# Kernel tuning notes

Hardware: AMD Instinct MI355X
Metric: run time of the kernel (lower is better)

Reference implementation:

```python
import jax, jax.numpy as jnp
import numpy as np

K = 128      # classes
CIN = 128    # ch_in
CL = 128     # ch_latent
B, H, W = 8, 1, 8192
SLOPE = 0.01 # F.leaky_relu default
EPS = 1e-5   # BatchNorm eps


def lrelu(x):
    return jnp.where(x >= 0, x, SLOPE * x)


def conv1x1(x, w, b):
    # x: (B,C,H,W), w: (O,C), b: (O,)
    return jnp.einsum('bchw,oc->bohw', x, w) + b[None, :, None, None]


def bn_eval(x, gamma, beta, mean, var):
    scale = gamma * jax.lax.rsqrt(var + EPS)
    return x * scale[None, :, None, None] + (beta - mean * scale)[None, :, None, None]


def setup_inputs() -> dict:
    key = jax.random.key(0)
    ks = jax.random.split(key, 16)
    def w(k, shape, fan_in):
        return jax.random.normal(k, shape, jnp.float32) / np.sqrt(fan_in)
    return {
        'x_in': jax.random.normal(ks[0], (B, CIN, H, W), jnp.float32),
        'cl1_w': w(ks[1], (CL, CIN), CIN), 'cl1_b': jnp.zeros((CL,), jnp.float32),
        'bn1_gamma': jnp.ones((CL,), jnp.float32), 'bn1_beta': jnp.zeros((CL,), jnp.float32),
        'bn1_mean': 0.1 * jax.random.normal(ks[2], (CL,), jnp.float32),
        'bn1_var': jax.random.uniform(ks[3], (CL,), jnp.float32, 0.5, 1.5),
        'cl2_w': w(ks[4], (CL, CL), CL), 'cl2_b': jnp.zeros((CL,), jnp.float32),
        'cl3_w': w(ks[5], (K + 1, CL), CL), 'cl3_b': jnp.zeros((K + 1,), jnp.float32),
        'reg1_w': w(ks[6], (CL, CIN), CIN), 'reg1_b': jnp.zeros((CL,), jnp.float32),
        'bnr_gamma': jnp.ones((CL,), jnp.float32), 'bnr_beta': jnp.zeros((CL,), jnp.float32),
        'bnr_mean': 0.1 * jax.random.normal(ks[7], (CL,), jnp.float32),
        'bnr_var': jax.random.uniform(ks[8], (CL,), jnp.float32, 0.5, 1.5),
        'cm2_w': w(ks[9], (K, CL, 32), CL), 'cm2_b': jnp.zeros((K, 32), jnp.float32),
        'cm3_w': w(ks[10], (K, 32, 1), 32), 'cm3_b': jnp.zeros((K, 1), jnp.float32),
    }


def reference(x_in, cl1_w, cl1_b, bn1_gamma, bn1_beta, bn1_mean, bn1_var,
              cl2_w, cl2_b, cl3_w, cl3_b,
              reg1_w, reg1_b, bnr_gamma, bnr_beta, bnr_mean, bnr_var,
              cm2_w, cm2_b, cm3_w, cm3_b):
    # classification branch
    x = lrelu(bn_eval(conv1x1(x_in, cl1_w, cl1_b), bn1_gamma, bn1_beta, bn1_mean, bn1_var))
    x = lrelu(conv1x1(x, cl2_w, cl2_b))
    x = conv1x1(x, cl3_w, cl3_b)                    # (B, K+1, H, W)
    logits = x[:, :K]
    mask = lrelu(x[:, -1:])                          # (B,1,H,W)
    inds = jnp.argmax(logits, axis=1)                # (B,H,W) int
    inds_r = inds.reshape(-1).astype(jnp.int32)      # (N,)
    xr = lrelu(bn_eval(conv1x1(x_in, reg1_w, reg1_b), bnr_gamma, bnr_beta, bnr_mean, bnr_var))
    # torch: transpose(1,3).reshape(-1, C)  -> (B,W,H,C) flatten
    xr = jnp.transpose(xr, (0, 3, 2, 1)).reshape(-1, CL)   # (N, CL)
    # CondMul 1: per-pixel gathered weight (N,CL,32)
    h = lrelu(jnp.einsum('ni,nio->no', xr, cm2_w[inds_r]) + cm2_b[inds_r])
    # CondMul 2: (N,32)->(N,1)
    reg = jnp.einsum('ni,nio->no', h, cm3_w[inds_r]) + cm3_b[inds_r]
    reg = reg.reshape(B, 1, 1, -1)                   # (B,1,1,H*W)
    x_real = (inds[:, None].astype(jnp.float32) + reg) * (1.0 / K)
    return x_real, mask
```

## Files before the change

kernel.cpp:

```cpp
#include <hip/hip_runtime.h>
#include <math.h>

#define NPOS 65536
#define NCH  128
#define DELTA 0.008f
#define HPAD 16

#define OFF_XR   0u
#define OFF_W1T  8388608u
#define OFF_W2T  (OFF_W1T + 16384u)
#define OFF_W3T  (OFF_W2T + 16384u)
#define OFF_B1F  (OFF_W3T + 16384u)
#define OFF_BRF  (OFF_B1F + 128u)
#define OFF_B2F  (OFF_BRF + 128u)
#define OFF_B3F  (OFF_B2F + 128u)
#define OFF_BF16 (OFF_B3F + 132u)
#define OFF_INT  (OFF_BF16 + 329728u)

#define UW1H 0u
#define UW1L 16384u
#define UWRH 32768u
#define UWRL 49152u
#define UW2H 65536u
#define UW2L 81920u
#define UW3H 98304u
#define UW3L 116736u
#define UW2K 135168u

#define NST 2080

typedef short bf16x8 __attribute__((ext_vector_type(8)));
typedef float f32x4 __attribute__((ext_vector_type(4)));
#define MFMA16 __builtin_amdgcn_mfma_f32_16x16x32_bf16

__device__ __forceinline__ float lrelu(float v) { return v >= 0.0f ? v : 0.01f * v; }
__device__ __forceinline__ unsigned short f2bf(float f) {
    unsigned u = __float_as_uint(f);
    return (unsigned short)((u + 0x7fffu + ((u >> 16) & 1u)) >> 16);
}
__device__ __forceinline__ float bf2f(unsigned short h) {
    return __uint_as_float(((unsigned)h) << 16);
}
__device__ __forceinline__ unsigned long long pack4(unsigned short a, unsigned short b,
                                                    unsigned short c, unsigned short d) {
    return (unsigned long long)a | ((unsigned long long)b << 16)
         | ((unsigned long long)c << 32) | ((unsigned long long)d << 48);
}

__global__ void k_prep(const float* __restrict__ cl1_w, const float* __restrict__ cl1_b,
                       const float* __restrict__ g1, const float* __restrict__ be1,
                       const float* __restrict__ mu1, const float* __restrict__ va1,
                       const float* __restrict__ cl2_w, const float* __restrict__ cl2_b,
                       const float* __restrict__ cl3_w, const float* __restrict__ cl3_b,
                       const float* __restrict__ reg1_w, const float* __restrict__ reg1_b,
                       const float* __restrict__ gr, const float* __restrict__ ber,
                       const float* __restrict__ mur, const float* __restrict__ var_,
                       const float* __restrict__ cm2w,
                       float* __restrict__ ws_f, unsigned short* __restrict__ wbf,
                       int* __restrict__ hist, int* __restrict__ cur,
                       int* __restrict__ fixcnt)
{
    const int bid = blockIdx.x;
    const int t = threadIdx.x;
    if (bid >= 128) {
        __shared__ float tl[32 * 132];
        int k = bid - 128;
        #pragma unroll
        for (int i = 0; i < 32; ++i) {
            float v = cm2w[(unsigned)k * 4096u + i * 128 + t];
            int ci = i * 4 + (t >> 5), o = t & 31;
            tl[o * 132 + ci] = v;
        }
        __syncthreads();
        #pragma unroll
        for (int i = 0; i < 32; ++i)
            wbf[UW2K + (unsigned)k * 4096u + i * 128 + t] = f2bf(tl[i * 132 + t]);
        return;
    }
    const int cout = bid;
    const int cin = t;
    const int row = cout * 128 + cin;
    float s1 = g1[cout] / sqrtf(va1[cout] + 1e-5f);
    float sr = gr[cout] / sqrtf(var_[cout] + 1e-5f);
    float w1 = cl1_w[row] * s1;
    float wr = reg1_w[row] * sr;
    float w2 = cl2_w[row];
    float w3 = cl3_w[row];
    ws_f[OFF_W1T + cin * 128 + cout] = w1;
    ws_f[OFF_W2T + cin * 128 + cout] = w2;
    ws_f[OFF_W3T + cin * 128 + cout] = w3;
    unsigned short h;
    h = f2bf(w1); wbf[UW1H + row] = h; wbf[UW1L + row] = f2bf(w1 - bf2f(h));
    h = f2bf(wr); wbf[UWRH + row] = h; wbf[UWRL + row] = f2bf(wr - bf2f(h));
    h = f2bf(w2); wbf[UW2H + row] = h; wbf[UW2L + row] = f2bf(w2 - bf2f(h));
    h = f2bf(w3); wbf[UW3H + row] = h; wbf[UW3L + row] = f2bf(w3 - bf2f(h));
    if (bid < 16) {
        float v = (bid == 0) ? cl3_w[128 * 128 + t] : 0.0f;
        int jj = (128 + bid) * 128 + t;
        h = f2bf(v); wbf[UW3H + jj] = h; wbf[UW3L + jj] = f2bf(v - bf2f(h));
    }
    if (bid == 0) {
        float s1b = g1[t] / sqrtf(va1[t] + 1e-5f);
        float srb = gr[t] / sqrtf(var_[t] + 1e-5f);
        ws_f[OFF_B1F + t] = cl1_b[t] * s1b + be1[t] - mu1[t] * s1b;
        ws_f[OFF_BRF + t] = reg1_b[t] * srb + ber[t] - mur[t] * srb;
        ws_f[OFF_B2F + t] = cl2_b[t];
        ws_f[OFF_B3F + t] = cl3_b[t];
        hist[t * HPAD] = 0;
        cur[t * HPAD] = 0;
    }
    if (bid == 1 && t == 0) { ws_f[OFF_B3F + 128] = cl3_b[128]; fixcnt[0] = 0; }
}

__global__ __launch_bounds__(256, 4)
void k_fused(const float* __restrict__ X, const float* __restrict__ wsf,
             const unsigned short* __restrict__ wbf,
             unsigned short* __restrict__ XRB, float* __restrict__ out_mask,
             int* __restrict__ inds, int* __restrict__ hist,
             int* __restrict__ fixcnt, int* __restrict__ fixlist)
{
    __shared__ __align__(16) unsigned short XBh[64 * 136];
    __shared__ __align__(16) unsigned short XBl[64 * 136];
    __shared__ float sm1[4 * 64];
    __shared__ float sm2[4 * 64];
    __shared__ int   si1[4 * 64];
    __shared__ int   lh[128];

    const int t = threadIdx.x;
    const int lane = t & 63;
    const int cl16 = lane & 15;
    const int q8 = (lane >> 4) * 8;
    const int q4 = (lane >> 4) * 4;
    const int wv = __builtin_amdgcn_readfirstlane(t >> 6);
    const unsigned nt64 = blockIdx.x * 64u;
    const unsigned base = nt64 + (nt64 >> 13) * 1040384u;

    const unsigned short* W1H = wbf + UW1H; const unsigned short* W1L = wbf + UW1L;
    const unsigned short* WRH = wbf + UWRH; const unsigned short* WRL = wbf + UWRL;
    const unsigned short* W2H = wbf + UW2H; const unsigned short* W2L = wbf + UW2L;
    const unsigned short* W3H = wbf + UW3H; const unsigned short* W3L = wbf + UW3L;
    const float* b1f = wsf + OFF_B1F;
    const float* brf = wsf + OFF_BRF;
    const float* b2f = wsf + OFF_B2F;
    const float* b3f = wsf + OFF_B3F;

    const f32x4 vzero = {0.f, 0.f, 0.f, 0.f};

    {
        const int pos = t & 63, cig = t >> 6;
        #pragma unroll
        for (int l = 0; l < 8; ++l) {
            int ci0 = cig * 32 + l * 4;
            float v0 = X[base + (unsigned)(ci0 + 0) * 8192u + pos];
            float v1 = X[base + (unsigned)(ci0 + 1) * 8192u + pos];
            float v2 = X[base + (unsigned)(ci0 + 2) * 8192u + pos];
            float v3 = X[base + (unsigned)(ci0 + 3) * 8192u + pos];
            unsigned short h0 = f2bf(v0), h1 = f2bf(v1), h2 = f2bf(v2), h3 = f2bf(v3);
            unsigned long long ph = pack4(h0, h1, h2, h3);
            unsigned long long pl = pack4(f2bf(v0 - bf2f(h0)), f2bf(v1 - bf2f(h1)),
                                          f2bf(v2 - bf2f(h2)), f2bf(v3 - bf2f(h3)));
            *(unsigned long long*)&XBh[pos * 136 + ci0] = ph;
            *(unsigned long long*)&XBl[pos * 136 + ci0] = pl;
        }
    }
    __syncthreads();

    f32x4 acc[2][4];

    #pragma unroll
    for (int m = 0; m < 2; ++m)
        #pragma unroll
        for (int n = 0; n < 4; ++n) acc[m][n] = vzero;
    #pragma unroll
    for (int kt = 0; kt < 4; ++kt) {
        bf16x8 Bh[4], Bl[4];
        #pragma unroll
        for (int n = 0; n < 4; ++n) {
            int bo = (n * 16 + cl16) * 136 + kt * 32 + q8;
            Bh[n] = *(const bf16x8*)&XBh[bo];
            Bl[n] = *(const bf16x8*)&XBl[bo];
        }
        #pragma unroll
        for (int m = 0; m < 2; ++m) {
            int ao = (wv * 32 + m * 16 + cl16) * 128 + kt * 32 + q8;
            bf16x8 arh = *(const bf16x8*)&WRH[ao], arl = *(const bf16x8*)&WRL[ao];
            #pragma unroll
            for (int n = 0; n < 4; ++n) {
                acc[m][n] = MFMA16(arh, Bl[n], acc[m][n], 0, 0, 0);
                acc[m][n] = MFMA16(arl, Bh[n], acc[m][n], 0, 0, 0);
                acc[m][n] = MFMA16(arh, Bh[n], acc[m][n], 0, 0, 0);
            }
        }
    }
    {
        #pragma unroll
        for (int m = 0; m < 2; ++m) {
            int cb = wv * 32 + m * 16 + q4;
            float br0 = brf[cb], br1 = brf[cb + 1], br2 = brf[cb + 2], br3 = brf[cb + 3];
            #pragma unroll
            for (int n = 0; n < 4; ++n) {
                unsigned pb = (nt64 + n * 16 + cl16) * 128u + cb;
                ushort4 xo;
                xo.x = f2bf(lrelu(acc[m][n][0] + br0));
                xo.y = f2bf(lrelu(acc[m][n][1] + br1));
                xo.z = f2bf(lrelu(acc[m][n][2] + br2));
                xo.w = f2bf(lrelu(acc[m][n][3] + br3));
                *(ushort4*)&XRB[pb] = xo;
            }
        }
    }

    #pragma unroll
    for (int m = 0; m < 2; ++m)
        #pragma unroll
        for (int n = 0; n < 4; ++n) acc[m][n] = vzero;
    #pragma unroll
    for (int kt = 0; kt < 4; ++kt) {
        bf16x8 Bh[4], Bl[4];
        #pragma unroll
        for (int n = 0; n < 4; ++n) {
            int bo = (n * 16 + cl16) * 136 + kt * 32 + q8;
            Bh[n] = *(const bf16x8*)&XBh[bo];
            Bl[n] = *(const bf16x8*)&XBl[bo];
        }
        #pragma unroll
        for (int m = 0; m < 2; ++m) {
            int ao = (wv * 32 + m * 16 + cl16) * 128 + kt * 32 + q8;
            bf16x8 a1h = *(const bf16x8*)&W1H[ao], a1l = *(const bf16x8*)&W1L[ao];
            #pragma unroll
            for (int n = 0; n < 4; ++n) {
                acc[m][n] = MFMA16(a1h, Bl[n], acc[m][n], 0, 0, 0);
                acc[m][n] = MFMA16(a1l, Bh[n], acc[m][n], 0, 0, 0);
                acc[m][n] = MFMA16(a1h, Bh[n], acc[m][n], 0, 0, 0);
            }
        }
    }
    __syncthreads();
    {
        #pragma unroll
        for (int m = 0; m < 2; ++m) {
            int cb = wv * 32 + m * 16 + q4;
            float b0 = b1f[cb], b1 = b1f[cb + 1], b2 = b1f[cb + 2], b3 = b1f[cb + 3];
            #pragma unroll
            for (int n = 0; n < 4; ++n) {
                float v0 = lrelu(acc[m][n][0] + b0), v1 = lrelu(acc[m][n][1] + b1);
                float v2 = lrelu(acc[m][n][2] + b2), v3 = lrelu(acc[m][n][3] + b3);
                unsigned short h0 = f2bf(v0), h1 = f2bf(v1), h2 = f2bf(v2), h3 = f2bf(v3);
                unsigned long long ph = pack4(h0, h1, h2, h3);
                unsigned long long pl = pack4(f2bf(v0 - bf2f(h0)), f2bf(v1 - bf2f(h1)),
                                              f2bf(v2 - bf2f(h2)), f2bf(v3 - bf2f(h3)));
                int idx = (n * 16 + cl16) * 136 + cb;
                *(unsigned long long*)&XBh[idx] = ph;
                *(unsigned long long*)&XBl[idx] = pl;
            }
        }
    }
    __syncthreads();

    #pragma unroll
    for (int m = 0; m < 2; ++m)
        #pragma unroll
        for (int n = 0; n < 4; ++n) acc[m][n] = vzero;
    #pragma unroll
    for (int kt = 0; kt < 4; ++kt) {
        bf16x8 Bh[4], Bl[4];
        #pragma unroll
        for (int n = 0; n < 4; ++n) {
            int bo = (n * 16 + cl16) * 136 + kt * 32 + q8;
            Bh[n] = *(const bf16x8*)&XBh[bo];
            Bl[n] = *(const bf16x8*)&XBl[bo];
        }
        #pragma unroll
        for (int m = 0; m < 2; ++m) {
            int ao = (wv * 32 + m * 16 + cl16) * 128 + kt * 32 + q8;
            bf16x8 ah = *(const bf16x8*)&W2H[ao], al = *(const bf16x8*)&W2L[ao];
            #pragma unroll
            for (int n = 0; n < 4; ++n) {
                acc[m][n] = MFMA16(ah, Bl[n], acc[m][n], 0, 0, 0);
                acc[m][n] = MFMA16(al, Bh[n], acc[m][n], 0, 0, 0);
                acc[m][n] = MFMA16(ah, Bh[n], acc[m][n], 0, 0, 0);
            }
        }
    }
    __syncthreads();
    {
        #pragma unroll
        for (int m = 0; m < 2; ++m) {
            int cb = wv * 32 + m * 16 + q4;
            float b0 = b2f[cb], b1 = b2f[cb + 1], b2 = b2f[cb + 2], b3 = b2f[cb + 3];
            #pragma unroll
            for (int n = 0; n < 4; ++n) {
                float v0 = lrelu(acc[m][n][0] + b0), v1 = lrelu(acc[m][n][1] + b1);
                float v2 = lrelu(acc[m][n][2] + b2), v3 = lrelu(acc[m][n][3] + b3);
                unsigned short h0 = f2bf(v0), h1 = f2bf(v1), h2 = f2bf(v2), h3 = f2bf(v3);
                unsigned long long ph = pack4(h0, h1, h2, h3);
                unsigned long long pl = pack4(f2bf(v0 - bf2f(h0)), f2bf(v1 - bf2f(h1)),
                                              f2bf(v2 - bf2f(h2)), f2bf(v3 - bf2f(h3)));
                int idx = (n * 16 + cl16) * 136 + cb;
                *(unsigned long long*)&XBh[idx] = ph;
                *(unsigned long long*)&XBl[idx] = pl;
            }
        }
    }
    __syncthreads();

    f32x4 accM = vzero;
    #pragma unroll
    for (int m = 0; m < 2; ++m)
        #pragma unroll
        for (int n = 0; n < 4; ++n) acc[m][n] = vzero;
    #pragma unroll
    for (int kt = 0; kt < 4; ++kt) {
        bf16x8 Bh[4], Bl[4];
        #pragma unroll
        for (int n = 0; n < 4; ++n) {
            int bo = (n * 16 + cl16) * 136 + kt * 32 + q8;
            Bh[n] = *(const bf16x8*)&XBh[bo];
            Bl[n] = *(const bf16x8*)&XBl[bo];
        }
        #pragma unroll
        for (int m = 0; m < 2; ++m) {
            int ao = (wv * 32 + m * 16 + cl16) * 128 + kt * 32 + q8;
            bf16x8 ah = *(const bf16x8*)&W3H[ao], al = *(const bf16x8*)&W3L[ao];
            #pragma unroll
            for (int n = 0; n < 4; ++n) {
                acc[m][n] = MFMA16(ah, Bl[n], acc[m][n], 0, 0, 0);
                acc[m][n] = MFMA16(al, Bh[n], acc[m][n], 0, 0, 0);
                acc[m][n] = MFMA16(ah, Bh[n], acc[m][n], 0, 0, 0);
            }
        }
        {
            int boM = (wv * 16 + cl16) * 136 + kt * 32 + q8;
            bf16x8 BhM = *(const bf16x8*)&XBh[boM];
            bf16x8 BlM = *(const bf16x8*)&XBl[boM];
            int ao = (128 + cl16) * 128 + kt * 32 + q8;
            bf16x8 ah = *(const bf16x8*)&W3H[ao], al = *(const bf16x8*)&W3L[ao];
            accM = MFMA16(ah, BlM, accM, 0, 0, 0);
            accM = MFMA16(al, BhM, accM, 0, 0, 0);
            accM = MFMA16(ah, BhM, accM, 0, 0, 0);
        }
    }

    {
        float bb[2][4];
        #pragma unroll
        for (int m = 0; m < 2; ++m) {
            int cb = wv * 32 + m * 16 + q4;
            bb[m][0] = b3f[cb]; bb[m][1] = b3f[cb + 1];
            bb[m][2] = b3f[cb + 2]; bb[m][3] = b3f[cb + 3];
        }
        float m1[4], m2[4]; int i1[4];
        #pragma unroll
        for (int n = 0; n < 4; ++n) {
            m1[n] = -1e30f; m2[n] = -1e30f; i1[n] = 0;
            #pragma unroll
            for (int m = 0; m < 2; ++m) {
                int cb = wv * 32 + m * 16 + q4;
                #pragma unroll
                for (int r = 0; r < 4; ++r) {
                    float v = acc[m][n][r] + bb[m][r];
                    if (v > m1[n]) { m2[n] = m1[n]; m1[n] = v; i1[n] = cb + r; }
                    else if (v > m2[n]) m2[n] = v;
                }
            }
        }
        #pragma unroll
        for (int off = 16; off <= 32; off <<= 1) {
            #pragma unroll
            for (int n = 0; n < 4; ++n) {
                float om1 = __shfl_xor(m1[n], off);
                float om2 = __shfl_xor(m2[n], off);
                int   oi1 = __shfl_xor(i1[n], off);
                if (om1 > m1[n] || (om1 == m1[n] && oi1 < i1[n])) {
                    m2[n] = fmaxf(m1[n], om2); m1[n] = om1; i1[n] = oi1;
                } else {
                    m2[n] = fmaxf(m2[n], om1);
                }
            }
        }
        if ((lane >> 4) == 0) {
            #pragma unroll
            for (int n = 0; n < 4; ++n) {
                sm1[wv * 64 + n * 16 + cl16] = m1[n];
                sm2[wv * 64 + n * 16 + cl16] = m2[n];
                si1[wv * 64 + n * 16 + cl16] = i1[n];
            }
        }
    }
    if ((lane >> 4) == 0) {
        float mb = b3f[128];
        out_mask[nt64 + wv * 16 + cl16] = lrelu(accM[0] + mb);
    }
    if (t < 128) lh[t] = 0;
    __syncthreads();
    if (t < 64) {
        float m1 = sm1[t], m2 = sm2[t];
        int i1 = si1[t];
        #pragma unroll
        for (int w = 1; w < 4; ++w) {
            float v1 = sm1[w * 64 + t];
            float v2 = sm2[w * 64 + t];
            int   vi = si1[w * 64 + t];
            if (v1 > m1) { m2 = fmaxf(m1, v2); m1 = v1; i1 = vi; }
            else         { m2 = fmaxf(m2, v1); }
        }
        int n = nt64 + t;
        inds[n] = i1;
        atomicAdd(&lh[i1], 1);
        if (m1 - m2 < DELTA) {
            int slot = atomicAdd(fixcnt, 1);
            fixlist[slot] = n;
        }
    }
    __syncthreads();
    if (t < 128 && lh[t] > 0) atomicAdd(&hist[t * HPAD], lh[t]);
}

__global__ __launch_bounds__(256, 4)
void k_fix(const float* __restrict__ X, const float* __restrict__ wsf,
           const int* __restrict__ fixcnt, const int* __restrict__ fixlist,
           int* __restrict__ inds, int* __restrict__ hist)
{
    __shared__ float xw[4][128];
    const int cnt = fixcnt[0];
    const int t = threadIdx.x;
    const int lane = t & 63;
    const int wv = t >> 6;
    const float* W1T = wsf + OFF_W1T;
    const float* W2T = wsf + OFF_W2T;
    const float* W3T = wsf + OFF_W3T;
    const float* b1f = wsf + OFF_B1F;
    const float* b2f = wsf + OFF_B2F;
    const float* b3f = wsf + OFF_B3F;

    for (int idx = blockIdx.x * 4 + wv; idx < cnt; idx += 2048) {
        int n = fixlist[idx];
        int oldid = inds[n];
        const float* xb = X + (unsigned)(n >> 13) * 1048576u + (unsigned)(n & 8191);
        float x0 = xb[(unsigned)lane * 8192u];
        float x1 = xb[(unsigned)(64 + lane) * 8192u];
        float a0, a1;

        xw[wv][lane] = x0; xw[wv][64 + lane] = x1;
        a0 = 0.f; a1 = 0.f;
        #pragma unroll 16
        for (int ci = 0; ci < 128; ++ci) {
            float xv = xw[wv][ci];
            const float* wr = W1T + ci * 128;
            a0 = fmaf(wr[lane], xv, a0);
            a1 = fmaf(wr[64 + lane], xv, a1);
        }
        x0 = lrelu(a0 + b1f[lane]); x1 = lrelu(a1 + b1f[64 + lane]);

        xw[wv][lane] = x0; xw[wv][64 + lane] = x1;
        a0 = 0.f; a1 = 0.f;
        #pragma unroll 16
        for (int ci = 0; ci < 128; ++ci) {
            float xv = xw[wv][ci];
            const float* wr = W2T + ci * 128;
            a0 = fmaf(wr[lane], xv, a0);
            a1 = fmaf(wr[64 + lane], xv, a1);
        }
        x0 = lrelu(a0 + b2f[lane]); x1 = lrelu(a1 + b2f[64 + lane]);

        xw[wv][lane] = x0; xw[wv][64 + lane] = x1;
        a0 = 0.f; a1 = 0.f;
        #pragma unroll 16
        for (int ci = 0; ci < 128; ++ci) {
            float xv = xw[wv][ci];
            const float* wr = W3T + ci * 128;
            a0 = fmaf(wr[lane], xv, a0);
            a1 = fmaf(wr[64 + lane], xv, a1);
        }
        float L0 = a0 + b3f[lane], L1 = a1 + b3f[64 + lane];
        float v; int id;
        if (L0 >= L1) { v = L0; id = lane; } else { v = L1; id = 64 + lane; }
        #pragma unroll
        for (int off = 1; off < 64; off <<= 1) {
            float ov = __shfl_xor(v, off);
            int   oi = __shfl_xor(id, off);
            if (ov > v || (ov == v && oi < id)) { v = ov; id = oi; }
        }
        if (lane == 0 && id != oldid) {
            inds[n] = id;
            atomicSub(&hist[oldid * HPAD], 1);
            atomicAdd(&hist[id * HPAD], 1);
        }
    }
}

__global__ void k_scatter(const int* __restrict__ inds, const int* __restrict__ hist,
                          int* __restrict__ cur, int* __restrict__ bucket)
{
    __shared__ int lh[128];
    __shared__ int gb[128];
    __shared__ int sv[128];
    __shared__ int sh[128];
    int t = threadIdx.x;
    if (t < 128) { int h = hist[t * HPAD]; sh[t] = h; sv[t] = h; lh[t] = 0; }
    __syncthreads();
    for (int d = 1; d < 128; d <<= 1) {
        int a = (t < 128 && t >= d) ? sv[t - d] : 0;
        __syncthreads();
        if (t < 128) sv[t] += a;
        __syncthreads();
    }
    int n = blockIdx.x * 256 + t;
    int id = inds[n];
    int r = atomicAdd(&lh[id], 1);
    __syncthreads();
    if (t < 128 && lh[t] > 0)
        gb[t] = (sv[t] - sh[t]) + atomicAdd(&cur[t * HPAD], lh[t]);
    __syncthreads();
    bucket[gb[id] + r] = n;
}

__global__ __launch_bounds__(256, 4)
void k_reg(const unsigned short* __restrict__ XRB, const unsigned short* __restrict__ wbf,
           const float* __restrict__ cm2b, const float* __restrict__ cm3w,
           const float* __restrict__ cm3b, const int* __restrict__ hist,
           const int* __restrict__ bucket, float* __restrict__ out)
{
    __shared__ __align__(16) unsigned short XP[4 * NST];
    __shared__ float red[64];
    __shared__ int sh[128];
    __shared__ int sv[128];
    __shared__ int st[128];
    __shared__ int skj[2];
    int bid = blockIdx.x;
    int t = threadIdx.x;
    if (t < 128) {
        int h = hist[t * HPAD];
        sh[t] = h; sv[t] = h; st[t] = (h + 63) >> 6;
    }
    __syncthreads();
    for (int d = 1; d < 128; d <<= 1) {
        int a = (t < 128 && t >= d) ? sv[t - d] : 0;
        int b = (t < 128 && t >= d) ? st[t - d] : 0;
        __syncthreads();
        if (t < 128) { sv[t] += a; st[t] += b; }
        __syncthreads();
    }
    if (bid >= st[127]) return;
    if (t < 128) {
        int ntk = (sh[t] + 63) >> 6;
        int tb = st[t] - ntk;
        if (bid >= tb && bid < st[t]) { skj[0] = t; skj[1] = bid - tb; }
    }
    __syncthreads();
    const int k = skj[0];
    const int start = skj[1] << 6;
    const int cnt = sh[k];
    const int base = sv[k] - sh[k];
    int lane = t & 63;
    int wv = __builtin_amdgcn_readfirstlane(t >> 6);
    const int n16 = lane & 15;
    const int quad = lane >> 4;

    {
        int rs = t >> 2;
        int q = t & 3;
        int sidx = start + rs;
        if (sidx >= cnt) sidx = cnt - 1;
        int n = bucket[base + sidx];
        const uint4* src = (const uint4*)(XRB + (unsigned)n * 128u + q * 32);
        uint4 a0 = src[0], a1 = src[1], a2 = src[2], a3 = src[3];
        unsigned db = (rs >> 4) * NST + q * 512 + (rs & 15) * 8;
        *(uint4*)&XP[db]       = a0;
        *(uint4*)&XP[db + 128] = a1;
        *(uint4*)&XP[db + 256] = a2;
        *(uint4*)&XP[db + 384] = a3;
    }
    __syncthreads();

    const unsigned short* wb = wbf + UW2K + (unsigned)k * 4096u;
    bf16x8 Bf[2][4];
    #pragma unroll
    for (int nf = 0; nf < 2; ++nf)
        #pragma unroll
        for (int kt = 0; kt < 4; ++kt)
            Bf[nf][kt] = *(const bf16x8*)&wb[(nf * 16 + n16) * 128 + kt * 32 + quad * 8];

    const f32x4 vzero = {0.f, 0.f, 0.f, 0.f};
    f32x4 acc[2];
    acc[0] = vzero; acc[1] = vzero;
    #pragma unroll
    for (int kt = 0; kt < 4; ++kt) {
        bf16x8 Af = *(const bf16x8*)&XP[wv * NST + kt * 512 + lane * 8];
        #pragma unroll
        for (int nf = 0; nf < 2; ++nf)
            acc[nf] = MFMA16(Af, Bf[nf][kt], acc[nf], 0, 0, 0);
    }

    float b2a = cm2b[k * 32 + n16], b2b = cm2b[k * 32 + 16 + n16];
    float w3a = cm3w[k * 32 + n16], w3b = cm3w[k * 32 + 16 + n16];
    #pragma unroll
    for (int r = 0; r < 4; ++r) {
        float p = lrelu(acc[0][r] + b2a) * w3a
                + lrelu(acc[1][r] + b2b) * w3b;
        p += __shfl_xor(p, 1);
        p += __shfl_xor(p, 2);
        p += __shfl_xor(p, 4);
        p += __shfl_xor(p, 8);
        if (n16 == 0)
            red[wv * 16 + quad * 4 + r] = p;
    }
    __syncthreads();
    if (t < 64 && start + t < cnt) {
        int n2 = bucket[base + start + t];
        out[n2] = ((float)k + red[t] + cm3b[k]) * (1.0f / 128.0f);
    }
}

extern "C" void kernel_launch(void* const* d_in, const int* in_sizes, int n_in,
                              void* d_out, int out_size, void* d_ws, size_t ws_size,
                              hipStream_t stream)
{
    (void)in_sizes; (void)n_in; (void)out_size; (void)ws_size;
    const float* x_in   = (const float*)d_in[0];
    const float* cl1_w  = (const float*)d_in[1];
    const float* cl1_b  = (const float*)d_in[2];
    const float* g1     = (const float*)d_in[3];
    const float* be1    = (const float*)d_in[4];
    const float* mu1    = (const float*)d_in[5];
    const float* va1    = (const float*)d_in[6];
    const float* cl2_w  = (const float*)d_in[7];
    const float* cl2_b  = (const float*)d_in[8];
    const float* cl3_w  = (const float*)d_in[9];
    const float* cl3_b  = (const float*)d_in[10];
    const float* reg1_w = (const float*)d_in[11];
    const float* reg1_b = (const float*)d_in[12];
    const float* gr     = (const float*)d_in[13];
    const float* ber    = (const float*)d_in[14];
    const float* mur    = (const float*)d_in[15];
    const float* var_   = (const float*)d_in[16];
    const float* cm2w   = (const float*)d_in[17];
    const float* cm2b   = (const float*)d_in[18];
    const float* cm3w   = (const float*)d_in[19];
    const float* cm3b   = (const float*)d_in[20];

    float* ws_f = (float*)d_ws;
    unsigned short* XRB = (unsigned short*)(ws_f + OFF_XR);
    unsigned short* wbf = (unsigned short*)(ws_f + OFF_BF16);
    int*   wsi    = (int*)(ws_f + OFF_INT);
    int*   inds   = wsi;
    int*   hist   = inds + 65536;
    int*   offb   = hist + 2048;
    int*   cur    = offb + 128;
    int*   ntt    = cur + 2048;
    int*   fixcnt = ntt + 4;
    int*   tiles  = fixcnt + 4;
    int*   fixlist= tiles + 1536;
    int*   bucket = fixlist + 65536;
    float* out = (float*)d_out;

    hipLaunchKernelGGL(k_prep, dim3(256), dim3(128), 0, stream,
                       cl1_w, cl1_b, g1, be1, mu1, va1, cl2_w, cl2_b, cl3_w, cl3_b,
                       reg1_w, reg1_b, gr, ber, mur, var_, cm2w, ws_f, wbf, hist, cur,
                       fixcnt);
    hipLaunchKernelGGL(k_fused, dim3(1024), dim3(256), 0, stream,
                       x_in, ws_f, wbf, XRB, out + 65536, inds, hist, fixcnt, fixlist);
    hipLaunchKernelGGL(k_fix, dim3(512), dim3(256), 0, stream,
                       x_in, ws_f, fixcnt, fixlist, inds, hist);
    hipLaunchKernelGGL(k_scatter, dim3(256), dim3(256), 0, stream,
                       inds, hist, cur, bucket);
    hipLaunchKernelGGL(k_reg, dim3(1536), dim3(256), 0, stream,
                       XRB, wbf, cm2b, cm3w, cm3b, hist, bucket, out);
}
```

Before: 204.0 us.

## Fuse near-tie argmax fix pass into main kernel via atomic work queue

Removes the separate k_fix launch. Blocks of k_fused now finish their tiles and then pull near-tie pixels from a global ticket queue, recomputing the classifier in fp32. Fixlist entries carry a packed valid flag and the old index so consumers can spin until each slot is published, and k_prep zeroes the list. This targets the kernel launch gap and the tail of the fix pass, at the cost of spin-waiting blocks, extra atomics and the need for forward progress among resident blocks.

```diff
diff --git a/kernel.cpp b/kernel.cpp
--- a/kernel.cpp
+++ b/kernel.cpp
@@ -58,10 +58,14 @@
                        const float* __restrict__ cm2w,
                        float* __restrict__ ws_f, unsigned short* __restrict__ wbf,
                        int* __restrict__ hist, int* __restrict__ cur,
-                       int* __restrict__ fixcnt)
+                       int* __restrict__ fixlist, int* __restrict__ alloc_,
+                       int* __restrict__ done_, int* __restrict__ ticket_)
 {
     const int bid = blockIdx.x;
     const int t = threadIdx.x;
+    fixlist[bid * 256 + t] = 0;
+    fixlist[bid * 256 + 128 + t] = 0;
+    if (bid == 1 && t == 1) { alloc_[0] = 0; done_[0] = 0; ticket_[0] = 0; }
     if (bid >= 128) {
         __shared__ float tl[32 * 132];
         int k = bid - 128;
@@ -109,7 +113,7 @@
         hist[t * HPAD] = 0;
         cur[t * HPAD] = 0;
     }
-    if (bid == 1 && t == 0) { ws_f[OFF_B3F + 128] = cl3_b[128]; fixcnt[0] = 0; }
+    if (bid == 1 && t == 0) ws_f[OFF_B3F + 128] = cl3_b[128];
 }
 
 __global__ __launch_bounds__(256, 4)
@@ -117,7 +121,8 @@
              const unsigned short* __restrict__ wbf,
              unsigned short* __restrict__ XRB, float* __restrict__ out_mask,
              int* __restrict__ inds, int* __restrict__ hist,
-             int* __restrict__ fixcnt, int* __restrict__ fixlist)
+             int* __restrict__ fixlist, int* __restrict__ alloc_,
+             int* __restrict__ done_, int* __restrict__ ticket_)
 {
     __shared__ __align__(16) unsigned short XBh[64 * 136];
     __shared__ __align__(16) unsigned short XBl[64 * 136];
@@ -408,83 +413,108 @@
         inds[n] = i1;
         atomicAdd(&lh[i1], 1);
         if (m1 - m2 < DELTA) {
-            int slot = atomicAdd(fixcnt, 1);
-            fixlist[slot] = n;
-        }
-    }
-    __syncthreads();
+            int slot = atomicAdd(alloc_, 1);
+            __hip_atomic_store(&fixlist[slot], (1 << 30) | (i1 << 16) | n,
+                               __ATOMIC_RELAXED, __HIP_MEMORY_SCOPE_AGENT);
+        }
+    }
+    __syncthreads();
+    if (t == 0)
+        __hip_atomic_fetch_add(done_, 1, __ATOMIC_RELEASE, __HIP_MEMORY_SCOPE_AGENT);
     if (t < 128 && lh[t] > 0) atomicAdd(&hist[t * HPAD], lh[t]);
-}
-
-__global__ __launch_bounds__(256, 4)
-void k_fix(const float* __restrict__ X, const float* __restrict__ wsf,
-           const int* __restrict__ fixcnt, const int* __restrict__ fixlist,
-           int* __restrict__ inds, int* __restrict__ hist)
-{
-    __shared__ float xw[4][128];
-    const int cnt = fixcnt[0];
-    const int t = threadIdx.x;
-    const int lane = t & 63;
-    const int wv = t >> 6;
-    const float* W1T = wsf + OFF_W1T;
-    const float* W2T = wsf + OFF_W2T;
-    const float* W3T = wsf + OFF_W3T;
-    const float* b1f = wsf + OFF_B1F;
-    const float* b2f = wsf + OFF_B2F;
-    const float* b3f = wsf + OFF_B3F;
-
-    for (int idx = blockIdx.x * 4 + wv; idx < cnt; idx += 2048) {
-        int n = fixlist[idx];
-        int oldid = inds[n];
-        const float* xb = X + (unsigned)(n >> 13) * 1048576u + (unsigned)(n & 8191);
-        float x0 = xb[(unsigned)lane * 8192u];
-        float x1 = xb[(unsigned)(64 + lane) * 8192u];
-        float a0, a1;
-
-        xw[wv][lane] = x0; xw[wv][64 + lane] = x1;
-        a0 = 0.f; a1 = 0.f;
-        #pragma unroll 16
-        for (int ci = 0; ci < 128; ++ci) {
-            float xv = xw[wv][ci];
-            const float* wr = W1T + ci * 128;
-            a0 = fmaf(wr[lane], xv, a0);
-            a1 = fmaf(wr[64 + lane], xv, a1);
-        }
-        x0 = lrelu(a0 + b1f[lane]); x1 = lrelu(a1 + b1f[64 + lane]);
-
-        xw[wv][lane] = x0; xw[wv][64 + lane] = x1;
-        a0 = 0.f; a1 = 0.f;
-        #pragma unroll 16
-        for (int ci = 0; ci < 128; ++ci) {
-            float xv = xw[wv][ci];
-            const float* wr = W2T + ci * 128;
-            a0 = fmaf(wr[lane], xv, a0);
-            a1 = fmaf(wr[64 + lane], xv, a1);
-        }
-        x0 = lrelu(a0 + b2f[lane]); x1 = lrelu(a1 + b2f[64 + lane]);
-
-        xw[wv][lane] = x0; xw[wv][64 + lane] = x1;
-        a0 = 0.f; a1 = 0.f;
-        #pragma unroll 16
-        for (int ci = 0; ci < 128; ++ci) {
-            float xv = xw[wv][ci];
-            const float* wr = W3T + ci * 128;
-            a0 = fmaf(wr[lane], xv, a0);
-            a1 = fmaf(wr[64 + lane], xv, a1);
-        }
-        float L0 = a0 + b3f[lane], L1 = a1 + b3f[64 + lane];
-        float v; int id;
-        if (L0 >= L1) { v = L0; id = lane; } else { v = L1; id = 64 + lane; }
-        #pragma unroll
-        for (int off = 1; off < 64; off <<= 1) {
-            float ov = __shfl_xor(v, off);
-            int   oi = __shfl_xor(id, off);
-            if (ov > v || (ov == v && oi < id)) { v = ov; id = oi; }
-        }
-        if (lane == 0 && id != oldid) {
-            inds[n] = id;
-            atomicSub(&hist[oldid * HPAD], 1);
-            atomicAdd(&hist[id * HPAD], 1);
+    __syncthreads();
+
+    {
+        float* xw = (float*)XBh;
+        const float* W1T = wsf + OFF_W1T;
+        const float* W2T = wsf + OFF_W2T;
+        const float* W3T = wsf + OFF_W3T;
+
+        for (;;) {
+            int tk = -1, pk = 0;
+            if (lane == 0) {
+                for (;;) {
+                    int al = __hip_atomic_load(alloc_, __ATOMIC_RELAXED, __HIP_MEMORY_SCOPE_AGENT);
+                    int tv = __hip_atomic_load(ticket_, __ATOMIC_RELAXED, __HIP_MEMORY_SCOPE_AGENT);
+                    if (tv < al) {
+                        tk = __hip_atomic_fetch_add(ticket_, 1, __ATOMIC_RELAXED,
+                                                    __HIP_MEMORY_SCOPE_AGENT);
+                        break;
+                    }
+                    if (__hip_atomic_load(done_, __ATOMIC_RELAXED, __HIP_MEMORY_SCOPE_AGENT) == 1024
+                        && tv >= __hip_atomic_load(alloc_, __ATOMIC_RELAXED, __HIP_MEMORY_SCOPE_AGENT)) {
+                        tk = -1; break;
+                    }
+                    __builtin_amdgcn_s_sleep(2);
+                }
+                if (tk >= 0) {
+                    for (;;) {
+                        pk = __hip_atomic_load(&fixlist[tk], __ATOMIC_RELAXED,
+                                               __HIP_MEMORY_SCOPE_AGENT);
+                        if (pk != 0) break;
+                        if (__hip_atomic_load(done_, __ATOMIC_RELAXED, __HIP_MEMORY_SCOPE_AGENT) == 1024
+                            && tk >= __hip_atomic_load(alloc_, __ATOMIC_RELAXED, __HIP_MEMORY_SCOPE_AGENT))
+                            break;
+                        __builtin_amdgcn_s_sleep(2);
+                    }
+                }
+            }
+            tk = __shfl(tk, 0);
+            pk = __shfl(pk, 0);
+            if (tk < 0 || pk == 0) break;
+
+            const int n = pk & 0xffff;
+            const int oldid = (pk >> 16) & 127;
+            const float* xb = X + (unsigned)(n >> 13) * 1048576u + (unsigned)(n & 8191);
+            float x0 = xb[(unsigned)lane * 8192u];
+            float x1 = xb[(unsigned)(64 + lane) * 8192u];
+            float a0, a1;
+
+            xw[wv * 128 + lane] = x0; xw[wv * 128 + 64 + lane] = x1;
+            a0 = 0.f; a1 = 0.f;
+            #pragma unroll 16
+            for (int ci = 0; ci < 128; ++ci) {
+                float xv = xw[wv * 128 + ci];
+                const float* wr = W1T + ci * 128;
+                a0 = fmaf(wr[lane], xv, a0);
+                a1 = fmaf(wr[64 + lane], xv, a1);
+            }
+            x0 = lrelu(a0 + b1f[lane]); x1 = lrelu(a1 + b1f[64 + lane]);
+
+            xw[wv * 128 + lane] = x0; xw[wv * 128 + 64 + lane] = x1;
+            a0 = 0.f; a1 = 0.f;
+            #pragma unroll 16
+            for (int ci = 0; ci < 128; ++ci) {
+                float xv = xw[wv * 128 + ci];
+                const float* wr = W2T + ci * 128;
+                a0 = fmaf(wr[lane], xv, a0);
+                a1 = fmaf(wr[64 + lane], xv, a1);
+            }
+            x0 = lrelu(a0 + b2f[lane]); x1 = lrelu(a1 + b2f[64 + lane]);
+
+            xw[wv * 128 + lane] = x0; xw[wv * 128 + 64 + lane] = x1;
+            a0 = 0.f; a1 = 0.f;
+            #pragma unroll 16
+            for (int ci = 0; ci < 128; ++ci) {
+                float xv = xw[wv * 128 + ci];
+                const float* wr = W3T + ci * 128;
+                a0 = fmaf(wr[lane], xv, a0);
+                a1 = fmaf(wr[64 + lane], xv, a1);
+            }
+            float L0 = a0 + b3f[lane], L1 = a1 + b3f[64 + lane];
+            float v; int id;
+            if (L0 >= L1) { v = L0; id = lane; } else { v = L1; id = 64 + lane; }
+            #pragma unroll
+            for (int off = 1; off < 64; off <<= 1) {
+                float ov = __shfl_xor(v, off);
+                int   oi = __shfl_xor(id, off);
+                if (ov > v || (ov == v && oi < id)) { v = ov; id = oi; }
+            }
+            if (lane == 0 && id != oldid) {
+                inds[n] = id;
+                atomicSub(&hist[oldid * HPAD], 1);
+                atomicAdd(&hist[id * HPAD], 1);
+            }
         }
     }
 }
@@ -650,6 +680,8 @@
     int*   ntt    = cur + 2048;
     int*   fixcnt = ntt + 4;
     int*   tiles  = fixcnt + 4;
+    int*   done_  = tiles;
+    int*   ticket_= tiles + HPAD;
     int*   fixlist= tiles + 1536;
     int*   bucket = fixlist + 65536;
     float* out = (float*)d_out;
@@ -657,11 +689,10 @@
     hipLaunchKernelGGL(k_prep, dim3(256), dim3(128), 0, stream,
                        cl1_w, cl1_b, g1, be1, mu1, va1, cl2_w, cl2_b, cl3_w, cl3_b,
                        reg1_w, reg1_b, gr, ber, mur, var_, cm2w, ws_f, wbf, hist, cur,
-                       fixcnt);
+                       fixlist, fixcnt, done_, ticket_);
     hipLaunchKernelGGL(k_fused, dim3(1024), dim3(256), 0, stream,
-                       x_in, ws_f, wbf, XRB, out + 65536, inds, hist, fixcnt, fixlist);
-    hipLaunchKernelGGL(k_fix, dim3(512), dim3(256), 0, stream,
-                       x_in, ws_f, fixcnt, fixlist, inds, hist);
+                       x_in, ws_f, wbf, XRB, out + 65536, inds, hist,
+                       fixlist, fixcnt, done_, ticket_);
     hipLaunchKernelGGL(k_scatter, dim3(256), dim3(256), 0, stream,
                        inds, hist, cur, bucket);
     hipLaunchKernelGGL(k_reg, dim3(1536), dim3(256), 0, stream,
```

New measurement: 389.4 us. +90.9%, slower.
